# Performance work log

Hardware: AMD Instinct MI355X
Metric: run time of the kernel (lower is better)

The kernel has to match this reference:

```python
import jax, jax.numpy as jnp
import numpy as np

N_NODES = 50000
N_EDGES = 800000
IN_DIM = 128
OUT_DIM = 64


def setup_inputs() -> dict:
    key = jax.random.key(0)
    k1, k2, k3, k4, k5 = jax.random.split(key, 5)
    h = jax.random.normal(k1, (N_NODES, IN_DIM), dtype=jnp.float32)
    # Xavier-normal-ish scale for weights
    W_w = jax.random.normal(k2, (IN_DIM, OUT_DIM), dtype=jnp.float32) * (2.0 / (IN_DIM + OUT_DIM)) ** 0.5
    W_b = jnp.zeros((OUT_DIM,), dtype=jnp.float32)
    A_w = jax.random.normal(k3, (2 * OUT_DIM, 1), dtype=jnp.float32) * (2.0 / (2 * OUT_DIM + 1)) ** 0.5
    A_b = jnp.zeros((1,), dtype=jnp.float32)
    src = jax.random.randint(k4, (N_EDGES,), 0, N_NODES, dtype=jnp.int32)
    dst = jax.random.randint(k5, (N_EDGES,), 0, N_NODES, dtype=jnp.int32)
    return {"h": h, "W_w": W_w, "W_b": W_b, "A_w": A_w, "A_b": A_b, "src": src, "dst": dst}


def reference(h, W_w, W_b, A_w, A_b, src, dst):
    n = h.shape[0]
    # Node projection: Wh = W(h)
    Wh = h @ W_w + W_b  # [N, D]
    # Attention logit e_ij = LeakyReLU(A([Wh_i; Wh_j])), computed as node-level
    # partial scores gathered per edge (same math as concat-linear, far less traffic).
    a_dst = (Wh @ A_w[:OUT_DIM, 0])  # [N] -> contribution of Wh_i (dst)
    a_src = (Wh @ A_w[OUT_DIM:, 0])  # [N] -> contribution of Wh_j (src)
    e = jax.nn.leaky_relu(a_dst[dst] + a_src[src] + A_b[0], negative_slope=0.2)  # [E]
    # Segment softmax over incoming edges of each destination node (stable).
    m = jax.ops.segment_max(e, dst, num_segments=n)  # [N], -inf for isolated nodes
    m = jnp.where(jnp.isfinite(m), m, 0.0)
    ex = jnp.exp(e - m[dst])  # [E]
    den = jax.ops.segment_sum(ex, dst, num_segments=n)  # [N]
    alpha = ex / den[dst]  # [E]
    # Weighted scatter-sum aggregate: h_i = sum_j alpha_ij * Wh_j
    out = jax.ops.segment_sum(alpha[:, None] * Wh[src], dst, num_segments=n)  # [N, D]
    # Dropout (p=0.6) is identity in eval mode; omitted for determinism.
    return out
```

## Files before the change

### kernel.cpp

```cpp
#include <hip/hip_runtime.h>
#include <hip/hip_bf16.h>
#include <hip/hip_fp16.h>

#define IN_DIM 128
#define OUT_DIM 64
#define MAXDEG 64

typedef __attribute__((ext_vector_type(8))) short short8v;
typedef __attribute__((ext_vector_type(4))) float float4v;
typedef unsigned short ushort_t;
typedef unsigned int uint_t;

__device__ inline ushort_t f_to_bf16(float f) {
    uint_t x = __float_as_uint(f);
    uint_t r = (x + 0x7fffu + ((x >> 16) & 1u)) >> 16;
    return (ushort_t)r;
}

__global__ __launch_bounds__(256) void gat_proj(
    const float* __restrict__ h, const float* __restrict__ W,
    const float* __restrict__ Wb, const float* __restrict__ Aw,
    ushort_t* __restrict__ Whb, float* __restrict__ a_dst_arr,
    float* __restrict__ a_src_arr, int* __restrict__ cnt, int N)
{
    __shared__ ushort_t Wl[16 * 64 * 8];

    const int t = threadIdx.x;

    for (int i = (int)blockIdx.x * 256 + t; i < N; i += (int)gridDim.x * 256)
        cnt[i] = 0;

    {
        int f = t * 32;
        #pragma unroll
        for (int i = 0; i < 32; i++, f++) {
            int frag = f >> 9;
            int lane = (f >> 3) & 63;
            int j    = f & 7;
            int k    = (frag >> 2) * 32 + (lane >> 4) * 8 + j;
            int d    = (frag & 3) * 16 + (lane & 15);
            Wl[f] = f_to_bf16(W[k * OUT_DIM + d]);
        }
    }
    __syncthreads();

    const int wave  = t >> 6;
    const int lane  = t & 63;
    const int node0 = ((int)blockIdx.x * 4 + wave) * 16;
    if (node0 >= N) return;
    const int quad = lane >> 4;
    const int col  = lane & 15;

    const int rowc = min(node0 + col, N - 1);
    const float* __restrict__ arow = h + (size_t)rowc * IN_DIM;

    float4v acc[4];
    #pragma unroll
    for (int db = 0; db < 4; db++) acc[db] = (float4v){0.f, 0.f, 0.f, 0.f};

    #pragma unroll
    for (int kb = 0; kb < 4; kb++) {
        const float* ap = arow + kb * 32 + quad * 8;
        float4 a0 = *(const float4*)ap;
        float4 a1 = *(const float4*)(ap + 4);
        union { short8v v; ushort_t u[8]; } af;
        af.u[0] = f_to_bf16(a0.x); af.u[1] = f_to_bf16(a0.y);
        af.u[2] = f_to_bf16(a0.z); af.u[3] = f_to_bf16(a0.w);
        af.u[4] = f_to_bf16(a1.x); af.u[5] = f_to_bf16(a1.y);
        af.u[6] = f_to_bf16(a1.z); af.u[7] = f_to_bf16(a1.w);
        #pragma unroll
        for (int db = 0; db < 4; db++) {
            short8v bf = *(const short8v*)&Wl[(((kb << 2) | db) * 64 + lane) * 8];
            acc[db] = __builtin_amdgcn_mfma_f32_16x16x32_bf16(af.v, bf, acc[db], 0, 0, 0);
        }
    }

    float wbv[4], awd[4], aws[4];
    #pragma unroll
    for (int db = 0; db < 4; db++) {
        wbv[db] = Wb[db * 16 + col];
        awd[db] = Aw[db * 16 + col];
        aws[db] = Aw[OUT_DIM + db * 16 + col];
    }

    float pd[4] = {0.f, 0.f, 0.f, 0.f};
    float ps[4] = {0.f, 0.f, 0.f, 0.f};
    #pragma unroll
    for (int db = 0; db < 4; db++) {
        #pragma unroll
        for (int r = 0; r < 4; r++) {
            float v = acc[db][r] + wbv[db];
            int node = node0 + quad * 4 + r;
            if (node < N)
                Whb[(size_t)node * OUT_DIM + db * 16 + col] = f_to_bf16(v);
            pd[r] = fmaf(v, awd[db], pd[r]);
            ps[r] = fmaf(v, aws[db], ps[r]);
        }
    }
    #pragma unroll
    for (int r = 0; r < 4; r++) {
        float d_ = pd[r], s_ = ps[r];
        #pragma unroll
        for (int off = 1; off < 16; off <<= 1) {
            d_ += __shfl_xor(d_, off);
            s_ += __shfl_xor(s_, off);
        }
        int node = node0 + quad * 4 + r;
        if (col == 0 && node < N) {
            a_dst_arr[node] = d_;
            a_src_arr[node] = s_;
        }
    }
}

__global__ __launch_bounds__(256) void gat_scatter(
    const int* __restrict__ src, const int* __restrict__ dst,
    const float* __restrict__ a_dst_arr, const float* __restrict__ a_src_arr,
    const float* __restrict__ Ab,
    int* __restrict__ cnt, uint_t* __restrict__ csr, int E)
{
    int base = (int)(blockIdx.x * blockDim.x + threadIdx.x) * 4;
    float ab = Ab[0];
    if (base + 4 <= E) {
        int4 s4 = *(const int4*)&src[base];
        int4 t4 = *(const int4*)&dst[base];
        int ss[4] = {s4.x, s4.y, s4.z, s4.w};
        int tt[4] = {t4.x, t4.y, t4.z, t4.w};
        #pragma unroll
        for (int i = 0; i < 4; i++) {
            float v = a_dst_arr[tt[i]] + a_src_arr[ss[i]] + ab;
            v = (v > 0.0f) ? v : 0.2f * v;
            float x = __expf(v);
            uint_t rec = (((uint_t)__half_as_ushort(__float2half(x))) << 16)
                       | (uint_t)(ss[i] & 0xffff);
            int r = atomicAdd(&cnt[tt[i]], 1);
            if (r < MAXDEG) csr[tt[i] * MAXDEG + r] = rec;
        }
    } else {
        for (int e = base; e < E; e++) {
            int s = src[e];
            int t = dst[e];
            float v = a_dst_arr[t] + a_src_arr[s] + ab;
            v = (v > 0.0f) ? v : 0.2f * v;
            float x = __expf(v);
            uint_t rec = (((uint_t)__half_as_ushort(__float2half(x))) << 16)
                       | (uint_t)(s & 0xffff);
            int r = atomicAdd(&cnt[t], 1);
            if (r < MAXDEG) csr[t * MAXDEG + r] = rec;
        }
    }
}

__global__ __launch_bounds__(256) void gat_agg(
    const int* __restrict__ cnt, const uint_t* __restrict__ csr,
    const uint_t* __restrict__ Whb2, float* __restrict__ out, int N)
{
    int node = (int)((blockIdx.x * blockDim.x + threadIdx.x) >> 6);
    int lane = threadIdx.x & 63;
    if (node >= N) return;
    int u   = __builtin_amdgcn_readfirstlane(node);
    int deg = min(cnt[u], MAXDEG);
    const uint_t* __restrict__ seg = csr + (size_t)u * MAXDEG;

    int   s_l = 0;
    float w_l = 0.f;
    if (lane < deg) {
        uint_t rec = seg[lane];
        s_l = (int)(rec & 0xffffu);
        w_l = __half2float(__ushort_as_half((ushort_t)(rec >> 16)));
    }
    float ws = w_l;
    #pragma unroll
    for (int off = 1; off < 64; off <<= 1) ws += __shfl_xor(ws, off);
    float inv  = (deg > 0) ? 1.0f / ws : 0.0f;
    float al_l = w_l * inv;

    const int el = lane >> 3;
    const int dl = lane & 7;

    float acc[8];
    #pragma unroll
    for (int i = 0; i < 8; i++) acc[i] = 0.f;

    for (int j = 0; j < deg; j += 16) {
        int   e0  = j + el;
        int   e1  = j + 8 + el;
        int   ss0 = __shfl(s_l, e0);
        float al0 = __shfl(al_l, e0);
        int   ss1 = __shfl(s_l, e1);
        float al1 = __shfl(al_l, e1);
        al0 = (e0 < deg) ? al0 : 0.0f;
        al1 = (e1 < deg) ? al1 : 0.0f;
        uint4 p0 = *(const uint4*)&Whb2[(size_t)ss0 * 32 + dl * 4];
        uint4 p1 = *(const uint4*)&Whb2[(size_t)ss1 * 32 + dl * 4];
        acc[0] = fmaf(al0, __uint_as_float(p0.x << 16),        acc[0]);
        acc[1] = fmaf(al0, __uint_as_float(p0.x & 0xffff0000u), acc[1]);
        acc[2] = fmaf(al0, __uint_as_float(p0.y << 16),        acc[2]);
        acc[3] = fmaf(al0, __uint_as_float(p0.y & 0xffff0000u), acc[3]);
        acc[4] = fmaf(al0, __uint_as_float(p0.z << 16),        acc[4]);
        acc[5] = fmaf(al0, __uint_as_float(p0.z & 0xffff0000u), acc[5]);
        acc[6] = fmaf(al0, __uint_as_float(p0.w << 16),        acc[6]);
        acc[7] = fmaf(al0, __uint_as_float(p0.w & 0xffff0000u), acc[7]);
        acc[0] = fmaf(al1, __uint_as_float(p1.x << 16),        acc[0]);
        acc[1] = fmaf(al1, __uint_as_float(p1.x & 0xffff0000u), acc[1]);
        acc[2] = fmaf(al1, __uint_as_float(p1.y << 16),        acc[2]);
        acc[3] = fmaf(al1, __uint_as_float(p1.y & 0xffff0000u), acc[3]);
        acc[4] = fmaf(al1, __uint_as_float(p1.z << 16),        acc[4]);
        acc[5] = fmaf(al1, __uint_as_float(p1.z & 0xffff0000u), acc[5]);
        acc[6] = fmaf(al1, __uint_as_float(p1.w << 16),        acc[6]);
        acc[7] = fmaf(al1, __uint_as_float(p1.w & 0xffff0000u), acc[7]);
    }

    #pragma unroll
    for (int off = 8; off < 64; off <<= 1) {
        #pragma unroll
        for (int i = 0; i < 8; i++) acc[i] += __shfl_xor(acc[i], off);
    }

    if (lane < 8) {
        float4 o0 = make_float4(acc[0], acc[1], acc[2], acc[3]);
        float4 o1 = make_float4(acc[4], acc[5], acc[6], acc[7]);
        *(float4*)&out[(size_t)u * OUT_DIM + dl * 8]     = o0;
        *(float4*)&out[(size_t)u * OUT_DIM + dl * 8 + 4] = o1;
    }
}

extern "C" void kernel_launch(void* const* d_in, const int* in_sizes, int n_in,
                              void* d_out, int out_size, void* d_ws, size_t ws_size,
                              hipStream_t stream)
{
    const float* h   = (const float*)d_in[0];
    const float* W_w = (const float*)d_in[1];
    const float* W_b = (const float*)d_in[2];
    const float* A_w = (const float*)d_in[3];
    const float* A_b = (const float*)d_in[4];
    const int*   src = (const int*)d_in[5];
    const int*   dst = (const int*)d_in[6];
    float* out = (float*)d_out;

    const int N = in_sizes[0] / IN_DIM;
    const int E = in_sizes[5];

    ushort_t* Whb   = (ushort_t*)d_ws;
    float* a_dst_a  = (float*)(Whb + (size_t)N * OUT_DIM);
    float* a_src_a  = a_dst_a + N;
    int*   cnt      = (int*)(a_src_a + N);
    uint_t* csr     = (uint_t*)(cnt + N);

    {
        int waves = (N + 15) / 16;
        int PB = (waves + 3) / 4;
        gat_proj<<<PB, 256, 0, stream>>>(h, W_w, W_b, A_w, Whb,
                                         a_dst_a, a_src_a, cnt, N);
    }
    {
        int grid = (E / 4 + 255) / 256;
        gat_scatter<<<grid, 256, 0, stream>>>(src, dst, a_dst_a, a_src_a,
                                              A_b, cnt, csr, E);
    }
    {
        int grid = (N + 3) / 4;
        gat_agg<<<grid, 256, 0, stream>>>(cnt, csr, (const uint_t*)Whb, out, N);
    }
}
```

Before: 157.4 us.

## Precompute attention scores via folded W·A, overlap edge scatter with projection

Attention scores are now computed in a separate lightweight pre-kernel by folding W·A into two 128-vectors, so each node's scores come from one dot product with h. The edge scatter and the MFMA projection that writes Wh are merged into one launch with disjoint block ranges, so the atomic-heavy scatter can overlap the GEMM. The cost is reading h twice (pre-kernel and projection) and keeping an extra kernel launch. Scores are computed in fp32 from h instead of from the bf16-rounded product, which slightly changes numerics.

```diff
diff --git a/kernel.cpp b/kernel.cpp
--- a/kernel.cpp
+++ b/kernel.cpp
@@ -17,19 +17,110 @@
     return (ushort_t)r;
 }
 
-__global__ __launch_bounds__(256) void gat_proj(
+__global__ __launch_bounds__(256) void gat_pre(
     const float* __restrict__ h, const float* __restrict__ W,
     const float* __restrict__ Wb, const float* __restrict__ Aw,
-    ushort_t* __restrict__ Whb, float* __restrict__ a_dst_arr,
-    float* __restrict__ a_src_arr, int* __restrict__ cnt, int N)
-{
-    __shared__ ushort_t Wl[16 * 64 * 8];
-
+    float* __restrict__ a_dst_arr, float* __restrict__ a_src_arr,
+    int* __restrict__ cnt, int N)
+{
+    __shared__ float vd[IN_DIM], vs[IN_DIM];
+    __shared__ float cc[2];
     const int t = threadIdx.x;
 
     for (int i = (int)blockIdx.x * 256 + t; i < N; i += (int)gridDim.x * 256)
         cnt[i] = 0;
 
+    if (t < IN_DIM) {
+        const float* wrow = W + t * OUT_DIM;
+        float sd = 0.f, ss = 0.f;
+        #pragma unroll 8
+        for (int d = 0; d < OUT_DIM; d++) {
+            float w = wrow[d];
+            sd = fmaf(w, Aw[d], sd);
+            ss = fmaf(w, Aw[OUT_DIM + d], ss);
+        }
+        vd[t] = sd; vs[t] = ss;
+    } else if (t == 128) {
+        float sd = 0.f, ss = 0.f;
+        for (int d = 0; d < OUT_DIM; d++) {
+            sd = fmaf(Wb[d], Aw[d], sd);
+            ss = fmaf(Wb[d], Aw[OUT_DIM + d], ss);
+        }
+        cc[0] = sd; cc[1] = ss;
+    }
+    __syncthreads();
+
+    const int ln  = t & 31;
+    const int sub = t >> 5;
+    for (int base = (int)blockIdx.x * 8; base < N; base += (int)gridDim.x * 8) {
+        int node = base + sub;
+        if (node < N) {
+            float4 hv  = *(const float4*)(h + (size_t)node * IN_DIM + ln * 4);
+            float4 vd4 = *(const float4*)&vd[ln * 4];
+            float4 vs4 = *(const float4*)&vs[ln * 4];
+            float pd = hv.x*vd4.x + hv.y*vd4.y + hv.z*vd4.z + hv.w*vd4.w;
+            float ps = hv.x*vs4.x + hv.y*vs4.y + hv.z*vs4.z + hv.w*vs4.w;
+            #pragma unroll
+            for (int off = 1; off < 32; off <<= 1) {
+                pd += __shfl_xor(pd, off);
+                ps += __shfl_xor(ps, off);
+            }
+            if (ln == 0) {
+                a_dst_arr[node] = pd + cc[0];
+                a_src_arr[node] = ps + cc[1];
+            }
+        }
+    }
+}
+
+__global__ __launch_bounds__(256) void gat_fused(
+    const float* __restrict__ h, const float* __restrict__ W,
+    const float* __restrict__ Wb,
+    ushort_t* __restrict__ Whb, int N,
+    const int* __restrict__ src, const int* __restrict__ dst,
+    const float* __restrict__ a_dst_arr, const float* __restrict__ a_src_arr,
+    const float* __restrict__ Ab,
+    int* __restrict__ cnt, uint_t* __restrict__ csr, int E, int HB)
+{
+    __shared__ ushort_t Wl[16 * 64 * 8];
+
+    const int t = threadIdx.x;
+
+    if ((int)blockIdx.x < HB) {
+        int base = ((int)blockIdx.x * 256 + t) * 4;
+        float ab = Ab[0];
+        if (base + 4 <= E) {
+            int4 s4 = *(const int4*)&src[base];
+            int4 t4 = *(const int4*)&dst[base];
+            int ss[4] = {s4.x, s4.y, s4.z, s4.w};
+            int tt[4] = {t4.x, t4.y, t4.z, t4.w};
+            #pragma unroll
+            for (int i = 0; i < 4; i++) {
+                float v = a_dst_arr[tt[i]] + a_src_arr[ss[i]] + ab;
+                v = (v > 0.0f) ? v : 0.2f * v;
+                float x = __expf(v);
+                uint_t rec = (((uint_t)__half_as_ushort(__float2half(x))) << 16)
+                           | (uint_t)(ss[i] & 0xffff);
+                int r = atomicAdd(&cnt[tt[i]], 1);
+                if (r < MAXDEG) csr[tt[i] * MAXDEG + r] = rec;
+            }
+        } else {
+            for (int e = base; e < E; e++) {
+                int s = src[e];
+                int d = dst[e];
+                float v = a_dst_arr[d] + a_src_arr[s] + ab;
+                v = (v > 0.0f) ? v : 0.2f * v;
+                float x = __expf(v);
+                uint_t rec = (((uint_t)__half_as_ushort(__float2half(x))) << 16)
+                           | (uint_t)(s & 0xffff);
+                int r = atomicAdd(&cnt[d], 1);
+                if (r < MAXDEG) csr[d * MAXDEG + r] = rec;
+            }
+        }
+        return;
+    }
+
+    const int pb = (int)blockIdx.x - HB;
     {
         int f = t * 32;
         #pragma unroll
@@ -46,7 +137,7 @@
 
     const int wave  = t >> 6;
     const int lane  = t & 63;
-    const int node0 = ((int)blockIdx.x * 4 + wave) * 16;
+    const int node0 = (pb * 4 + wave) * 16;
     if (node0 >= N) return;
     const int quad = lane >> 4;
     const int col  = lane & 15;
@@ -75,78 +166,15 @@
         }
     }
 
-    float wbv[4], awd[4], aws[4];
     #pragma unroll
     for (int db = 0; db < 4; db++) {
-        wbv[db] = Wb[db * 16 + col];
-        awd[db] = Aw[db * 16 + col];
-        aws[db] = Aw[OUT_DIM + db * 16 + col];
-    }
-
-    float pd[4] = {0.f, 0.f, 0.f, 0.f};
-    float ps[4] = {0.f, 0.f, 0.f, 0.f};
-    #pragma unroll
-    for (int db = 0; db < 4; db++) {
+        float wbv = Wb[db * 16 + col];
         #pragma unroll
         for (int r = 0; r < 4; r++) {
-            float v = acc[db][r] + wbv[db];
             int node = node0 + quad * 4 + r;
             if (node < N)
-                Whb[(size_t)node * OUT_DIM + db * 16 + col] = f_to_bf16(v);
-            pd[r] = fmaf(v, awd[db], pd[r]);
-            ps[r] = fmaf(v, aws[db], ps[r]);
-        }
-    }
-    #pragma unroll
-    for (int r = 0; r < 4; r++) {
-        float d_ = pd[r], s_ = ps[r];
-        #pragma unroll
-        for (int off = 1; off < 16; off <<= 1) {
-            d_ += __shfl_xor(d_, off);
-            s_ += __shfl_xor(s_, off);
-        }
-        int node = node0 + quad * 4 + r;
-        if (col == 0 && node < N) {
-            a_dst_arr[node] = d_;
-            a_src_arr[node] = s_;
-        }
-    }
-}
-
-__global__ __launch_bounds__(256) void gat_scatter(
-    const int* __restrict__ src, const int* __restrict__ dst,
-    const float* __restrict__ a_dst_arr, const float* __restrict__ a_src_arr,
-    const float* __restrict__ Ab,
-    int* __restrict__ cnt, uint_t* __restrict__ csr, int E)
-{
-    int base = (int)(blockIdx.x * blockDim.x + threadIdx.x) * 4;
-    float ab = Ab[0];
-    if (base + 4 <= E) {
-        int4 s4 = *(const int4*)&src[base];
-        int4 t4 = *(const int4*)&dst[base];
-        int ss[4] = {s4.x, s4.y, s4.z, s4.w};
-        int tt[4] = {t4.x, t4.y, t4.z, t4.w};
-        #pragma unroll
-        for (int i = 0; i < 4; i++) {
-            float v = a_dst_arr[tt[i]] + a_src_arr[ss[i]] + ab;
-            v = (v > 0.0f) ? v : 0.2f * v;
-            float x = __expf(v);
-            uint_t rec = (((uint_t)__half_as_ushort(__float2half(x))) << 16)
-                       | (uint_t)(ss[i] & 0xffff);
-            int r = atomicAdd(&cnt[tt[i]], 1);
-            if (r < MAXDEG) csr[tt[i] * MAXDEG + r] = rec;
-        }
-    } else {
-        for (int e = base; e < E; e++) {
-            int s = src[e];
-            int t = dst[e];
-            float v = a_dst_arr[t] + a_src_arr[s] + ab;
-            v = (v > 0.0f) ? v : 0.2f * v;
-            float x = __expf(v);
-            uint_t rec = (((uint_t)__half_as_ushort(__float2half(x))) << 16)
-                       | (uint_t)(s & 0xffff);
-            int r = atomicAdd(&cnt[t], 1);
-            if (r < MAXDEG) csr[t * MAXDEG + r] = rec;
+                Whb[(size_t)node * OUT_DIM + db * 16 + col] =
+                    f_to_bf16(acc[db][r] + wbv);
         }
     }
 }
@@ -248,15 +276,17 @@
     uint_t* csr     = (uint_t*)(cnt + N);
 
     {
+        int grid = (N + 7) / 8;
+        gat_pre<<<grid, 256, 0, stream>>>(h, W_w, W_b, A_w,
+                                          a_dst_a, a_src_a, cnt, N);
+    }
+    {
+        int HB = (E + 1023) / 1024;
         int waves = (N + 15) / 16;
         int PB = (waves + 3) / 4;
-        gat_proj<<<PB, 256, 0, stream>>>(h, W_w, W_b, A_w, Whb,
-                                         a_dst_a, a_src_a, cnt, N);
-    }
-    {
-        int grid = (E / 4 + 255) / 256;
-        gat_scatter<<<grid, 256, 0, stream>>>(src, dst, a_dst_a, a_src_a,
-                                              A_b, cnt, csr, E);
+        gat_fused<<<HB + PB, 256, 0, stream>>>(h, W_w, W_b, Whb, N,
+                                               src, dst, a_dst_a, a_src_a,
+                                               A_b, cnt, csr, E, HB);
     }
     {
         int grid = (N + 3) / 4;
```

After: 182.8 us. 16.1% more time.
